# Kernel optimization log

Hardware: AMD Instinct MI355X
Metric: run time of the kernel (lower is better)

Reference implementation:

```python
import jax, jax.numpy as jnp
import numpy as np

B, S, D = 4, 2048, 256
H = 8
HD = D // H
DFF = 512
EPS_CUTOFF = 1e-15
LN_EPS = 1e-5


def _layer_norm(x, gamma, beta):
    mu = jnp.mean(x, axis=-1, keepdims=True)
    var = jnp.mean(jnp.square(x - mu), axis=-1, keepdims=True)
    return (x - mu) * jax.lax.rsqrt(var + LN_EPS) * gamma + beta


def setup_inputs() -> dict:
    key = jax.random.key(0)
    ks = jax.random.split(key, 12)
    s = 1.0 / np.sqrt(D)
    inp = {
        "tokens": jax.random.normal(ks[0], (B, S, D), dtype=jnp.float32),
        "cutoff_factors": jax.random.uniform(ks[1], (B, S, S), dtype=jnp.float32),
        "Wqkv": jax.random.uniform(ks[2], (3 * D, D), jnp.float32, -s, s),
        "bqkv": jnp.zeros((3 * D,), jnp.float32),
        "Wo": jax.random.uniform(ks[3], (D, D), jnp.float32, -s, s),
        "bo": jnp.zeros((D,), jnp.float32),
        "ln1_g": jnp.ones((D,), jnp.float32),
        "ln1_b": jnp.zeros((D,), jnp.float32),
        "ln2_g": jnp.ones((D,), jnp.float32),
        "ln2_b": jnp.zeros((D,), jnp.float32),
        "W1": jax.random.uniform(ks[4], (DFF, D), jnp.float32, -s, s),
        "b1": jax.random.uniform(ks[5], (DFF,), jnp.float32, -s, s),
        "W2": jax.random.uniform(ks[6], (D, DFF), jnp.float32, -1.0 / np.sqrt(DFF), 1.0 / np.sqrt(DFF)),
        "b2": jax.random.uniform(ks[7], (D,), jnp.float32, -1.0 / np.sqrt(DFF), 1.0 / np.sqrt(DFF)),
        "use_manual_attention": 1,
    }
    return inp


def reference(tokens, cutoff_factors, Wqkv, bqkv, Wo, bo, ln1_g, ln1_b, ln2_g, ln2_b, W1, b1, W2, b2, use_manual_attention):
    # --- attention block ---
    qkv = tokens @ Wqkv.T + bqkv                      # [B,S,3D]
    qkv = qkv.reshape(B, S, 3, H, HD).transpose(2, 0, 3, 1, 4)  # [3,B,H,S,HD]
    q, k, v = qkv[0], qkv[1], qkv[2]
    attn_mask = jnp.log(jnp.clip(cutoff_factors, EPS_CUTOFF))[:, None, :, :]  # [B,1,S,S]
    scores = jnp.einsum("bhqd,bhkd->bhqk", q, k) / np.sqrt(HD) + attn_mask
    probs = jax.nn.softmax(scores, axis=-1)
    attn = jnp.einsum("bhqk,bhkd->bhqd", probs, v)    # [B,H,S,HD]
    attn = attn.transpose(0, 2, 1, 3).reshape(B, S, D)
    attn = attn @ Wo.T + bo
    # --- PostLN residual + norm ---
    x = _layer_norm(tokens + attn, ln1_g, ln1_b)
    # --- MLP (SiLU) ---
    h = jax.nn.silu(x @ W1.T + b1)
    mlp_out = h @ W2.T + b2
    return _layer_norm(x + mlp_out, ln2_g, ln2_b)
```

## Files before the change

### kernel.cpp

```cpp
#include <hip/hip_runtime.h>
#include <hip/hip_bf16.h>
#include <math.h>

#define B_ 4
#define S_ 2048
#define D_ 256
#define H_ 8
#define HD_ 32
#define DFF_ 512

typedef __attribute__((ext_vector_type(8))) short bf16x8;
typedef __attribute__((ext_vector_type(4))) float f32x4;

__device__ inline short f2bf(float f) {
  union { float f; unsigned u; } x; x.f = f;
  unsigned r = (x.u + 0x7FFFu + ((x.u >> 16) & 1u)) >> 16;
  return (short)r;
}
__device__ inline float bf2f(short s) {
  union { unsigned u; float f; } x; x.u = ((unsigned)(unsigned short)s) << 16;
  return x.f;
}
__device__ inline unsigned cvt_pk_bf16(float a, float b) {
  unsigned r;
  asm("v_cvt_pk_bf16_f32 %0, %1, %2" : "=v"(r) : "v"(a), "v"(b));
  return r;
}
__device__ inline float exp2v(float x) {
  float r;
  asm("v_exp_f32 %0, %1" : "=v"(r) : "v"(x));
  return r;
}

__global__ __launch_bounds__(256) void cvt_w(const float* __restrict__ wq,
                                             const float* __restrict__ wo, const float* __restrict__ w1,
                                             const float* __restrict__ w2,
                                             short* __restrict__ dwq,
                                             short* __restrict__ dwo, short* __restrict__ dw1,
                                             short* __restrict__ dw2) {
  int blk = blockIdx.x;
  const float* src; short* dst; int base;
  if (blk < 192)      { src = wq; dst = dwq; base = blk; }
  else if (blk < 256) { src = wo; dst = dwo; base = blk - 192; }
  else if (blk < 384) { src = w1; dst = dw1; base = blk - 256; }
  else                { src = w2; dst = dw2; base = blk - 384; }
  int i = (base * 256 + threadIdx.x) * 4;
  float4 v = *(const float4*)(src + i);
  short4 s; s.x = f2bf(v.x); s.y = f2bf(v.y); s.z = f2bf(v.z); s.w = f2bf(v.w);
  *(short4*)(dst + i) = s;
}

template<int MODE>
__global__ __launch_bounds__(256) void gemm_bf(const short* __restrict__ A,
                                               const float* __restrict__ Af,
                                               const short* __restrict__ W,
                                               const float* __restrict__ bias,
                                               short* __restrict__ Cb,
                                               unsigned* __restrict__ kmaxp,
                                               int M, int N, int K) {
  constexpr int BM = 128, BN = 64;
  __shared__ short As[BM][72];
  __shared__ short Bs[BN][72];
  const int tid = threadIdx.x;
  const int wid = tid >> 6, lane = tid & 63;
  const int g = lane >> 4, lc = lane & 15;
  const int wr = wid >> 1, wc = wid & 1;
  const int rowBase = blockIdx.y * BM;
  const int colBase = blockIdx.x * BN;

  f32x4 acc[4][2];
#pragma unroll
  for (int m = 0; m < 4; ++m)
#pragma unroll
    for (int n = 0; n < 2; ++n) { acc[m][n][0]=0.f; acc[m][n][1]=0.f; acc[m][n][2]=0.f; acc[m][n][3]=0.f; }

  for (int k0 = 0; k0 < K; k0 += 64) {
    __syncthreads();
#pragma unroll
    for (int i = 0; i < 4; ++i) {
      int task = tid + 256 * i;
      int r = task >> 3, c = (task & 7) * 8;
      if (MODE == 2) {
        const float* ap = Af + (size_t)(rowBase + r) * K + k0 + c;
        float4 v0 = *(const float4*)ap;
        float4 v1 = *(const float4*)(ap + 4);
        union { unsigned u[4]; bf16x8 v; } t;
        t.u[0] = cvt_pk_bf16(v0.x, v0.y);
        t.u[1] = cvt_pk_bf16(v0.z, v0.w);
        t.u[2] = cvt_pk_bf16(v1.x, v1.y);
        t.u[3] = cvt_pk_bf16(v1.z, v1.w);
        *(bf16x8*)&As[r][c] = t.v;
      } else {
        *(bf16x8*)&As[r][c] = *(const bf16x8*)(A + (size_t)(rowBase + r) * K + k0 + c);
      }
    }
#pragma unroll
    for (int i = 0; i < 2; ++i) {
      int task = tid + 256 * i;
      int r = task >> 3, c = (task & 7) * 8;
      *(bf16x8*)&Bs[r][c] = *(const bf16x8*)(W + (size_t)(colBase + r) * K + k0 + c);
    }
    __syncthreads();
#pragma unroll
    for (int ks = 0; ks < 2; ++ks) {
      bf16x8 af[4], bfr[2];
#pragma unroll
      for (int m = 0; m < 4; ++m) af[m] = *(const bf16x8*)&As[wr*64 + m*16 + lc][ks*32 + g*8];
#pragma unroll
      for (int n = 0; n < 2; ++n) bfr[n] = *(const bf16x8*)&Bs[wc*32 + n*16 + lc][ks*32 + g*8];
#pragma unroll
      for (int m = 0; m < 4; ++m)
#pragma unroll
        for (int n = 0; n < 2; ++n)
          acc[m][n] = __builtin_amdgcn_mfma_f32_16x16x32_bf16(af[m], bfr[n], acc[m][n], 0, 0, 0);
    }
  }

  const int part = (colBase + wc * 32) >> 8;
  float rmax = 0.f;
#pragma unroll
  for (int m = 0; m < 4; ++m) {
    float nsum[4] = {0.f, 0.f, 0.f, 0.f};
#pragma unroll
    for (int n = 0; n < 2; ++n) {
      int col = colBase + wc*32 + n*16 + lc;
      float bv = bias[col];
      int row0 = rowBase + wr*64 + m*16 + g*4;
      float vj[4];
#pragma unroll
      for (int j = 0; j < 4; ++j) vj[j] = acc[m][n][j] + bv;
      if (MODE == 1) {
#pragma unroll
        for (int j = 0; j < 4; ++j) {
          float v = vj[j];
          v = v / (1.f + __expf(-v));
          Cb[(size_t)(row0 + j) * N + col] = f2bf(v);
        }
      } else {
        int h = (col >> 5) & 7;
        int hd = col & 31;
        int b = row0 >> 11, s0 = row0 & 2047;
        if (part == 2) {
          short4 s4;
          s4.x = f2bf(vj[0]); s4.y = f2bf(vj[1]); s4.z = f2bf(vj[2]); s4.w = f2bf(vj[3]);
          *(short4*)(Cb + 2 * 2097152 + (((size_t)b * 8 + h) * 32 + hd) * 2048 + s0) = s4;
        } else {
          float sc = (part == 0) ? 0.25506807f : 1.f;
#pragma unroll
          for (int j = 0; j < 4; ++j)
            Cb[(size_t)part * 2097152 + (((size_t)b * 8 + h) * 2048 + s0 + j) * 32 + hd] = f2bf(vj[j] * sc);
          if (part == 1) {
#pragma unroll
            for (int j = 0; j < 4; ++j) nsum[j] = fmaf(vj[j], vj[j], nsum[j]);
          }
        }
      }
    }
    if (MODE == 2 && part == 1) {
#pragma unroll
      for (int j = 0; j < 4; ++j) {
        float t = nsum[j];
        t += __shfl_xor(t, 1, 64); t += __shfl_xor(t, 2, 64);
        t += __shfl_xor(t, 4, 64); t += __shfl_xor(t, 8, 64);
        rmax = fmaxf(rmax, t);
      }
    }
  }
  if (MODE == 2 && part == 1) {
    rmax = fmaxf(rmax, __shfl_xor(rmax, 16, 64));
    rmax = fmaxf(rmax, __shfl_xor(rmax, 32, 64));
    if (lane == 0) {
      int h = ((colBase + wc * 32) >> 5) & 7;
      int b = rowBase >> 11;
      atomicMax(kmaxp + b * 8 + h, __float_as_uint(rmax));
    }
  }
}

__global__ __launch_bounds__(256) void gemm_bf64(const short* __restrict__ A,
                                                 const short* __restrict__ W,
                                                 const float* __restrict__ bias,
                                                 float* __restrict__ Cf,
                                                 int M, int N, int K) {
  __shared__ short As[64][72];
  __shared__ short Bs[64][72];
  const int tid = threadIdx.x;
  const int wid = tid >> 6, lane = tid & 63;
  const int g = lane >> 4, lc = lane & 15;
  const int wr = wid >> 1, wc = wid & 1;
  const int rowBase = blockIdx.y * 64;
  const int colBase = blockIdx.x * 64;

  f32x4 acc[2][2];
#pragma unroll
  for (int m = 0; m < 2; ++m)
#pragma unroll
    for (int n = 0; n < 2; ++n) { acc[m][n][0]=0.f; acc[m][n][1]=0.f; acc[m][n][2]=0.f; acc[m][n][3]=0.f; }

  for (int k0 = 0; k0 < K; k0 += 64) {
    __syncthreads();
#pragma unroll
    for (int i = 0; i < 2; ++i) {
      int task = tid + 256 * i;
      int r = task >> 3, c = (task & 7) * 8;
      *(bf16x8*)&As[r][c] = *(const bf16x8*)(A + (size_t)(rowBase + r) * K + k0 + c);
      *(bf16x8*)&Bs[r][c] = *(const bf16x8*)(W + (size_t)(colBase + r) * K + k0 + c);
    }
    __syncthreads();
#pragma unroll
    for (int ks = 0; ks < 2; ++ks) {
      bf16x8 af[2], bfr[2];
#pragma unroll
      for (int m = 0; m < 2; ++m) af[m] = *(const bf16x8*)&As[wr*32 + m*16 + lc][ks*32 + g*8];
#pragma unroll
      for (int n = 0; n < 2; ++n) bfr[n] = *(const bf16x8*)&Bs[wc*32 + n*16 + lc][ks*32 + g*8];
#pragma unroll
      for (int m = 0; m < 2; ++m)
#pragma unroll
        for (int n = 0; n < 2; ++n)
          acc[m][n] = __builtin_amdgcn_mfma_f32_16x16x32_bf16(af[m], bfr[n], acc[m][n], 0, 0, 0);
    }
  }

#pragma unroll
  for (int m = 0; m < 2; ++m)
#pragma unroll
    for (int n = 0; n < 2; ++n) {
      int col = colBase + wc*32 + n*16 + lc;
      float bv = bias[col];
      int row0 = rowBase + wr*32 + m*16 + g*4;
#pragma unroll
      for (int j = 0; j < 4; ++j)
        Cf[(size_t)(row0 + j) * N + col] = acc[m][n][j] + bv;
    }
}

__global__ __launch_bounds__(256, 4) void attn_mfma(const short* __restrict__ qbf,
                                                    const short* __restrict__ kbf,
                                                    const short* __restrict__ vtbf,
                                                    const float* __restrict__ cutoff,
                                                    const unsigned* __restrict__ kmaxp,
                                                    short* __restrict__ outbf) {
  constexpr int KB = 64;
  const int qt = blockIdx.x & 31;
  const int h  = (blockIdx.x >> 5) & 7;
  const int b  = blockIdx.x >> 8;
  const int tid = threadIdx.x;
  const int wid = tid >> 6, lane = tid & 63;
  const int g = lane >> 4, lc = lane & 15;

  __shared__ __align__(16) short Ks[2][KB][32];
  __shared__ __align__(16) short Vt[2][HD_][72];
  __shared__ __align__(16) short Pq[4][16][72];

  const int bh = b * H_ + h;
  const int qrow = qt * 64 + wid * 16 + lc;
  const short* qg = qbf + (size_t)bh * S_ * HD_;
  const short* kg = kbf + (size_t)bh * S_ * HD_;
  const short* vg = vtbf + (size_t)bh * HD_ * S_;

  bf16x8 qf = *(const bf16x8*)(qg + (size_t)qrow * HD_ + g * 8);

  float ssq = 0.f;
#pragma unroll
  for (int i = 0; i < 8; ++i) { float f = bf2f(qf[i]); ssq = fmaf(f, f, ssq); }
  ssq += __shfl_xor(ssq, 16, 64);
  ssq += __shfl_xor(ssq, 32, 64);
  const float m = sqrtf(ssq * __uint_as_float(kmaxp[bh]));

  f32x4 oacc[2];
#pragma unroll
  for (int d = 0; d < 2; ++d) { oacc[d][0]=0.f; oacc[d][1]=0.f; oacc[d][2]=0.f; oacc[d][3]=0.f; }
  float sml = 0.f;

  const float* cb = cutoff + ((size_t)(b * S_) + qrow) * (size_t)S_;

  const int kr = tid >> 2;
  const int kslot = ((tid & 3) ^ ((kr >> 1) & 3)) * 8;
  const short* kptr = kg + (size_t)kr * HD_ + (tid & 3) * 8;
  const int vr = tid >> 3;
  const int vc = (tid & 7) * 8;
  const short* vptr = vg + (size_t)vr * S_ + vc;

  bf16x8 kreg = *(const bf16x8*)kptr;
  bf16x8 vreg = *(const bf16x8*)vptr;
  *(bf16x8*)&Ks[0][kr][kslot] = kreg;
  *(bf16x8*)&Vt[0][vr][vc] = vreg;
  float4 cvbuf[2][4];
#pragma unroll
  for (int t = 0; t < 4; ++t) cvbuf[0][t] = *(const float4*)(cb + t * 16 + g * 4);
#pragma unroll
  for (int t = 0; t < 4; ++t) cvbuf[1][t] = *(const float4*)(cb + KB + t * 16 + g * 4);
  __syncthreads();

  int cur = 0;
#pragma unroll 2
  for (int kt = 0; kt < S_; kt += KB) {
    const bool notlast = (kt + KB < S_);
    const int par = (kt >> 6) & 1;

    float4 cv[4];
#pragma unroll
    for (int t = 0; t < 4; ++t) cv[t] = cvbuf[par][t];
    if (kt + 2 * KB < S_) {
#pragma unroll
      for (int t = 0; t < 4; ++t)
        cvbuf[par][t] = *(const float4*)(cb + kt + 2 * KB + t * 16 + g * 4);
    }

    if (notlast) {
      kreg = *(const bf16x8*)(kptr + (size_t)(kt + KB) * HD_);
      vreg = *(const bf16x8*)(vptr + (kt + KB));
    }

    bf16x8 kf[4];
#pragma unroll
    for (int t = 0; t < 4; ++t)
      kf[t] = *(const bf16x8*)&Ks[cur][t*16 + lc][(g ^ ((lc >> 1) & 3)) * 8];
    f32x4 st[4];
#pragma unroll
    for (int t = 0; t < 4; ++t) {
      f32x4 z = {0.f, 0.f, 0.f, 0.f};
      st[t] = __builtin_amdgcn_mfma_f32_16x16x32_bf16(kf[t], qf, z, 0, 0, 0);
    }

#pragma unroll
    for (int t = 0; t < 4; ++t) {
      float p0 = cv[t].x * exp2v(fminf(st[t][0] - m, 8.f));
      float p1 = cv[t].y * exp2v(fminf(st[t][1] - m, 8.f));
      float p2 = cv[t].z * exp2v(fminf(st[t][2] - m, 8.f));
      float p3 = cv[t].w * exp2v(fminf(st[t][3] - m, 8.f));
      sml += (p0 + p1) + (p2 + p3);
      uint2 pk;
      pk.x = cvt_pk_bf16(p0, p1);
      pk.y = cvt_pk_bf16(p2, p3);
      *(uint2*)&Pq[wid][lc][t*16 + g*4] = pk;
    }

    asm volatile("s_waitcnt lgkmcnt(0)" ::: "memory");
    __builtin_amdgcn_sched_barrier(0);

#pragma unroll
    for (int kh = 0; kh < 2; ++kh) {
      bf16x8 pb = *(const bf16x8*)&Pq[wid][lc][kh*32 + g*8];
#pragma unroll
      for (int dh = 0; dh < 2; ++dh) {
        bf16x8 va = *(const bf16x8*)&Vt[cur][dh*16 + lc][kh*32 + g*8];
        oacc[dh] = __builtin_amdgcn_mfma_f32_16x16x32_bf16(va, pb, oacc[dh], 0, 0, 0);
      }
    }

    if (notlast) {
      __syncthreads();
      *(bf16x8*)&Ks[cur ^ 1][kr][kslot] = kreg;
      *(bf16x8*)&Vt[cur ^ 1][vr][vc] = vreg;
      __syncthreads();
      cur ^= 1;
    }
  }

  float s = sml;
  s += __shfl_xor(s, 16, 64);
  s += __shfl_xor(s, 32, 64);
  float inv = 1.f / s;
#pragma unroll
  for (int dh = 0; dh < 2; ++dh) {
    uint2 pk;
    pk.x = cvt_pk_bf16(oacc[dh][0] * inv, oacc[dh][1] * inv);
    pk.y = cvt_pk_bf16(oacc[dh][2] * inv, oacc[dh][3] * inv);
    *(uint2*)(outbf + ((size_t)(b * S_) + qrow) * D_ + h * HD_ + dh * 16 + g * 4) = pk;
  }
}

template<int WBF>
__global__ __launch_bounds__(256) void residual_ln(const float* __restrict__ xa,
                                                   const float* __restrict__ xb,
                                                   const float* __restrict__ g,
                                                   const float* __restrict__ bt,
                                                   float* __restrict__ out,
                                                   short* __restrict__ outbf) {
  const int row  = blockIdx.x * 4 + (threadIdx.x >> 6);
  const int lane = threadIdx.x & 63;
  float4 va = *(const float4*)(xa + (size_t)row * D_ + lane * 4);
  float4 vb = *(const float4*)(xb + (size_t)row * D_ + lane * 4);
  float v[4] = {va.x + vb.x, va.y + vb.y, va.z + vb.z, va.w + vb.w};
  float s = v[0] + v[1] + v[2] + v[3];
#pragma unroll
  for (int o = 32; o > 0; o >>= 1) s += __shfl_xor(s, o, 64);
  float mu = s * (1.f / D_);
  float var = 0.f;
#pragma unroll
  for (int i = 0; i < 4; ++i) { v[i] -= mu; var += v[i] * v[i]; }
#pragma unroll
  for (int o = 32; o > 0; o >>= 1) var += __shfl_xor(var, o, 64);
  float rs = rsqrtf(var * (1.f / D_) + 1e-5f);
  float4 g4 = *(const float4*)(g + lane * 4);
  float4 b4 = *(const float4*)(bt + lane * 4);
  float4 o4 = {v[0] * rs * g4.x + b4.x, v[1] * rs * g4.y + b4.y,
               v[2] * rs * g4.z + b4.z, v[3] * rs * g4.w + b4.w};
  *(float4*)(out + (size_t)row * D_ + lane * 4) = o4;
  if (WBF) {
    short4 s4; s4.x = f2bf(o4.x); s4.y = f2bf(o4.y); s4.z = f2bf(o4.z); s4.w = f2bf(o4.w);
    *(short4*)(outbf + (size_t)row * D_ + lane * 4) = s4;
  }
}

extern "C" void kernel_launch(void* const* d_in, const int* in_sizes, int n_in,
                              void* d_out, int out_size, void* d_ws, size_t ws_size,
                              hipStream_t stream) {
  const float* tokens = (const float*)d_in[0];
  const float* cutoff = (const float*)d_in[1];
  const float* Wqkv   = (const float*)d_in[2];
  const float* bqkv   = (const float*)d_in[3];
  const float* Wo     = (const float*)d_in[4];
  const float* bo     = (const float*)d_in[5];
  const float* ln1g   = (const float*)d_in[6];
  const float* ln1b   = (const float*)d_in[7];
  const float* ln2g   = (const float*)d_in[8];
  const float* ln2b   = (const float*)d_in[9];
  const float* W1     = (const float*)d_in[10];
  const float* b1     = (const float*)d_in[11];
  const float* W2     = (const float*)d_in[12];
  const float* b2     = (const float*)d_in[13];
  float* out = (float*)d_out;

  char* w = (char*)d_ws;
  const size_t MB = 1 << 20;
  short* qbf    = (short*)w;
  short* kbf    = qbf + 2097152;
  short* vtbf   = qbf + 2 * 2097152;
  short* attnbf = (short*)(w + 12 * MB);
  short* wq_bf  = (short*)(w + 16 * MB);
  short* wo_bf  = wq_bf + 196608;
  short* w1_bf  = wo_bf + 65536;
  short* w2_bf  = w1_bf + 131072;
  float* projOut = (float*)(w + 18 * MB);
  float* xbuf    = (float*)(w + 26 * MB);
  unsigned* kmax = (unsigned*)(w + 34 * MB);
  short* xbbf    = qbf;
  short* hbbf    = kbf;
  float* mlpOut  = projOut;

  const int M = B_ * S_;

  hipMemsetAsync(kmax, 0, 128, stream);
  cvt_w<<<dim3(512), 256, 0, stream>>>(Wqkv, Wo, W1, W2, wq_bf, wo_bf, w1_bf, w2_bf);

  gemm_bf<2><<<dim3(12, 64), 256, 0, stream>>>(nullptr, tokens, wq_bf, bqkv, qbf, kmax, M, 3 * D_, D_);
  attn_mfma<<<dim3(1024), 256, 0, stream>>>(qbf, kbf, vtbf, cutoff, kmax, attnbf);
  gemm_bf64<<<dim3(4, 128), 256, 0, stream>>>(attnbf, wo_bf, bo, projOut, M, D_, D_);
  residual_ln<1><<<dim3(M / 4), 256, 0, stream>>>(tokens, projOut, ln1g, ln1b, xbuf, xbbf);
  gemm_bf<1><<<dim3(8, 64), 256, 0, stream>>>(xbbf, nullptr, w1_bf, b1, hbbf, nullptr, M, DFF_, D_);
  gemm_bf64<<<dim3(4, 128), 256, 0, stream>>>(hbbf, w2_bf, b2, mlpOut, M, D_, DFF_);
  residual_ln<0><<<dim3(M / 4), 256, 0, stream>>>(xbuf, mlpOut, ln2g, ln2b, out, nullptr);
}
```

Baseline: 151.8 us.

## Load K/V fragments directly from global memory, dropping LDS staging and barriers

The attention kernel no longer stages K and V tiles through double-buffered shared memory with two __syncthreads per tile. Each wave now loads its MFMA K and V operand fragments straight from global memory, relying on L1/L2 reuse across waves. The cutoff prefetch pipeline is also dropped in favour of direct per-iteration loads, and the fmin clamp on the exponent is removed. Barriers and LDS traffic go away, but global load latency is no longer hidden by software prefetch, and each wave issues redundant loads for the same K/V data.

Result: slower. 222.8 us (+46.8%).

```diff
diff --git a/kernel.cpp b/kernel.cpp
--- a/kernel.cpp
+++ b/kernel.cpp
@@ -249,8 +249,6 @@
   const int wid = tid >> 6, lane = tid & 63;
   const int g = lane >> 4, lc = lane & 15;
 
-  __shared__ __align__(16) short Ks[2][KB][32];
-  __shared__ __align__(16) short Vt[2][HD_][72];
   __shared__ __align__(16) short Pq[4][16][72];
 
   const int bh = b * H_ + h;
@@ -274,49 +272,25 @@
   float sml = 0.f;
 
   const float* cb = cutoff + ((size_t)(b * S_) + qrow) * (size_t)S_;
-
-  const int kr = tid >> 2;
-  const int kslot = ((tid & 3) ^ ((kr >> 1) & 3)) * 8;
-  const short* kptr = kg + (size_t)kr * HD_ + (tid & 3) * 8;
-  const int vr = tid >> 3;
-  const int vc = (tid & 7) * 8;
-  const short* vptr = vg + (size_t)vr * S_ + vc;
-
-  bf16x8 kreg = *(const bf16x8*)kptr;
-  bf16x8 vreg = *(const bf16x8*)vptr;
-  *(bf16x8*)&Ks[0][kr][kslot] = kreg;
-  *(bf16x8*)&Vt[0][vr][vc] = vreg;
-  float4 cvbuf[2][4];
-#pragma unroll
-  for (int t = 0; t < 4; ++t) cvbuf[0][t] = *(const float4*)(cb + t * 16 + g * 4);
-#pragma unroll
-  for (int t = 0; t < 4; ++t) cvbuf[1][t] = *(const float4*)(cb + KB + t * 16 + g * 4);
-  __syncthreads();
-
-  int cur = 0;
+  const short* kfp = kg + (size_t)lc * HD_ + g * 8;
+  const short* vfp0 = vg + (size_t)lc * S_ + g * 8;
+  const short* vfp1 = vg + (size_t)(16 + lc) * S_ + g * 8;
+
 #pragma unroll 2
   for (int kt = 0; kt < S_; kt += KB) {
-    const bool notlast = (kt + KB < S_);
-    const int par = (kt >> 6) & 1;
-
+    bf16x8 kf[4];
+#pragma unroll
+    for (int t = 0; t < 4; ++t) kf[t] = *(const bf16x8*)(kfp + (size_t)(kt + t * 16) * HD_);
+    bf16x8 va[2][2];
+#pragma unroll
+    for (int kh = 0; kh < 2; ++kh) {
+      va[kh][0] = *(const bf16x8*)(vfp0 + kt + kh * 32);
+      va[kh][1] = *(const bf16x8*)(vfp1 + kt + kh * 32);
+    }
     float4 cv[4];
 #pragma unroll
-    for (int t = 0; t < 4; ++t) cv[t] = cvbuf[par][t];
-    if (kt + 2 * KB < S_) {
-#pragma unroll
-      for (int t = 0; t < 4; ++t)
-        cvbuf[par][t] = *(const float4*)(cb + kt + 2 * KB + t * 16 + g * 4);
-    }
-
-    if (notlast) {
-      kreg = *(const bf16x8*)(kptr + (size_t)(kt + KB) * HD_);
-      vreg = *(const bf16x8*)(vptr + (kt + KB));
-    }
-
-    bf16x8 kf[4];
-#pragma unroll
-    for (int t = 0; t < 4; ++t)
-      kf[t] = *(const bf16x8*)&Ks[cur][t*16 + lc][(g ^ ((lc >> 1) & 3)) * 8];
+    for (int t = 0; t < 4; ++t) cv[t] = *(const float4*)(cb + kt + t * 16 + g * 4);
+
     f32x4 st[4];
 #pragma unroll
     for (int t = 0; t < 4; ++t) {
@@ -326,10 +300,10 @@
 
 #pragma unroll
     for (int t = 0; t < 4; ++t) {
-      float p0 = cv[t].x * exp2v(fminf(st[t][0] - m, 8.f));
-      float p1 = cv[t].y * exp2v(fminf(st[t][1] - m, 8.f));
-      float p2 = cv[t].z * exp2v(fminf(st[t][2] - m, 8.f));
-      float p3 = cv[t].w * exp2v(fminf(st[t][3] - m, 8.f));
+      float p0 = cv[t].x * exp2v(st[t][0] - m);
+      float p1 = cv[t].y * exp2v(st[t][1] - m);
+      float p2 = cv[t].z * exp2v(st[t][2] - m);
+      float p3 = cv[t].w * exp2v(st[t][3] - m);
       sml += (p0 + p1) + (p2 + p3);
       uint2 pk;
       pk.x = cvt_pk_bf16(p0, p1);
@@ -344,18 +318,8 @@
     for (int kh = 0; kh < 2; ++kh) {
       bf16x8 pb = *(const bf16x8*)&Pq[wid][lc][kh*32 + g*8];
 #pragma unroll
-      for (int dh = 0; dh < 2; ++dh) {
-        bf16x8 va = *(const bf16x8*)&Vt[cur][dh*16 + lc][kh*32 + g*8];
-        oacc[dh] = __builtin_amdgcn_mfma_f32_16x16x32_bf16(va, pb, oacc[dh], 0, 0, 0);
-      }
-    }
-
-    if (notlast) {
-      __syncthreads();
-      *(bf16x8*)&Ks[cur ^ 1][kr][kslot] = kreg;
-      *(bf16x8*)&Vt[cur ^ 1][vr][vc] = vreg;
-      __syncthreads();
-      cur ^= 1;
+      for (int dh = 0; dh < 2; ++dh)
+        oacc[dh] = __builtin_amdgcn_mfma_f32_16x16x32_bf16(va[kh][dh], pb, oacc[dh], 0, 0, 0);
     }
   }
 
```
